# Optimization experiments

Hardware: AMD Instinct MI355X
Metric: run time of the kernel (lower is better)

Reference implementation:

```python
import jax, jax.numpy as jnp
import numpy as np
from jax import lax

_SIGMA = 1.5
_KSIZE = 5
_THRESH = 30.0
# TF rgb_to_grayscale luma weights
_RGB_W = np.array([0.2989, 0.5870, 0.1140], dtype=np.float32)

def _gauss1d():
    x = np.arange(_KSIZE, dtype=np.float32) - (_KSIZE - 1) / 2.0
    g = np.exp(-(x ** 2) / (2.0 * _SIGMA ** 2))
    return (g / g.sum()).astype(np.float32)

def _conv2d_same(x, k2d):
    # x: [B,H,W,1], k2d: [kh,kw]; reflect padding (TF image-op convention), valid conv
    kh, kw = k2d.shape
    ph, pw = kh // 2, kw // 2
    xp = jnp.pad(x, ((0, 0), (ph, ph), (pw, pw), (0, 0)), mode='reflect')
    k = k2d.reshape(kh, kw, 1, 1)
    return lax.conv_general_dilated(xp, k, window_strides=(1, 1), padding='VALID',
                                    dimension_numbers=('NHWC', 'HWIO', 'NHWC'))

def setup_inputs() -> dict:
    key = jax.random.key(0)
    inputs = jax.random.uniform(key, (32, 512, 512, 3), dtype=jnp.float32)
    return {"inputs": inputs}

def reference(inputs):
    # 1) grayscale
    gray = jnp.einsum('bhwc,c->bhw', inputs, jnp.asarray(_RGB_W))[..., None]  # [B,H,W,1]
    # 2) 5x5 gaussian blur (separable)
    g1 = jnp.asarray(_gauss1d())
    blurred = _conv2d_same(gray, g1[:, None])   # vertical pass [5,1]
    blurred = _conv2d_same(blurred, g1[None, :])  # horizontal pass [1,5]
    # 3) sobel x / y (3x3)
    kx = jnp.asarray(np.array([[-1, 0, 1], [-2, 0, 2], [-1, 0, 1]], dtype=np.float32))
    ky = jnp.asarray(np.array([[-1, -2, -1], [0, 0, 0], [1, 2, 1]], dtype=np.float32))
    sx = _conv2d_same(blurred, kx)
    sy = _conv2d_same(blurred, ky)
    # 4) magnitude + threshold (direction computed then unused in original; skipped)
    magnitude = jnp.sqrt(sx * sx + sy * sy)
    edges = jnp.where(magnitude > _THRESH, 1.0, 0.0).astype(inputs.dtype)
    return edges
```

## Files before the change

kernel.cpp:

```cpp
#include <hip/hip_runtime.h>

#define IMG_H 512
#define IMG_W 512
#define TILE  64
#define GR    70
#define GSTR  72
#define BR    66
#define BSTR  72
#define BLSTR 68

__device__ __forceinline__ int reflect(int i, int n) {
    i = (i < 0) ? -i : i;
    i = (i >= n) ? (2 * n - 2 - i) : i;
    return i;
}

__global__ __launch_bounds__(256)
void edge_fused_kernel(const float* __restrict__ in, float* __restrict__ out) {
    const int bx0 = blockIdx.x * TILE;
    const int by0 = blockIdx.y * TILE;
    const int b   = blockIdx.z;
    const int tx  = threadIdx.x;
    const int ty  = threadIdx.y;

    __shared__ float bufA[GR * GSTR];
    __shared__ float bufB[BR * BSTR];

    const float g0 = 0.12007839f;
    const float g1 = 0.23388075f;
    const float g2 = 0.29208172f;
    const float wr = 0.2989f, wg = 0.5870f, wb = 0.1140f;

    const float* img = in + (size_t)b * (IMG_H * IMG_W * 3);

    for (int i = ty; i < GR; i += 4) {
        const int gy = reflect(by0 - 3 + i, IMG_H);
        const float* row = img + (size_t)gy * (IMG_W * 3);
        for (int j = tx; j < GR; j += 64) {
            const int gx = reflect(bx0 - 3 + j, IMG_W);
            const float* p = row + gx * 3;
            bufA[i * GSTR + j] = p[0] * wr + p[1] * wg + p[2] * wb;
        }
    }
    __syncthreads();

    for (int i = ty; i < BR; i += 4) {
        for (int j = tx; j < GR; j += 64) {
            const float* c = &bufA[i * GSTR + j];
            bufB[i * BSTR + j] =
                g0 * (c[0] + c[4 * GSTR]) +
                g1 * (c[GSTR] + c[3 * GSTR]) +
                g2 * c[2 * GSTR];
        }
    }
    __syncthreads();

    for (int i = ty; i < BR; i += 4) {
        for (int j = tx; j < BR; j += 64) {
            const float* c = &bufB[i * BSTR + j];
            bufA[i * BLSTR + j] =
                g0 * (c[0] + c[4]) +
                g1 * (c[1] + c[3]) +
                g2 * c[2];
        }
    }
    __syncthreads();

    float* orow = out + (size_t)b * (IMG_H * IMG_W);
    for (int i = ty; i < TILE; i += 4) {
        const int oy = by0 + i;
        const int j = tx;
        const float* c = &bufA[(i + 1) * BLSTR + (j + 1)];
        const float tl = c[-BLSTR - 1], tc = c[-BLSTR], tr = c[-BLSTR + 1];
        const float ml = c[-1],                          mr = c[1];
        const float bl = c[BLSTR - 1],  bc = c[BLSTR],  br = c[BLSTR + 1];
        const float sx = (tr - tl) + 2.0f * (mr - ml) + (br - bl);
        const float sy = (bl - tl) + 2.0f * (bc - tc) + (br - tr);
        const float m2 = sx * sx + sy * sy;
        orow[(size_t)oy * IMG_W + bx0 + j] = (m2 > 900.0f) ? 1.0f : 0.0f;
    }
}

extern "C" void kernel_launch(void* const* d_in, const int* in_sizes, int n_in,
                              void* d_out, int out_size, void* d_ws, size_t ws_size,
                              hipStream_t stream) {
    const float* in = (const float*)d_in[0];
    float* out = (float*)d_out;
    const int B = in_sizes[0] / (IMG_H * IMG_W * 3);
    dim3 grid(IMG_W / TILE, IMG_H / TILE, B);
    dim3 block(64, 4, 1);
    edge_fused_kernel<<<grid, block, 0, stream>>>(in, out);
}
```

Before: 184.4 us.

## Vectorize fused edge kernel with float4 loads and smaller tiles

Replaces the scalar fused grayscale/blur/sobel kernel with a float4-vectorized version. Interior tiles load RGB with 128-bit global loads, the blur passes and the sobel stage use float4 shared-memory accesses, and the output is written as float4. Tiles shrink from 64x64 to 64x32 with a 1D block and a launch-bounds occupancy hint, which adds grid parallelism and raises the halo overhead. Edge tiles fall back to a scalar reflect path.

```diff
diff --git a/kernel.cpp b/kernel.cpp
--- a/kernel.cpp
+++ b/kernel.cpp
@@ -2,82 +2,122 @@
 
 #define IMG_H 512
 #define IMG_W 512
-#define TILE  64
-#define GR    70
-#define GSTR  72
-#define BR    66
-#define BSTR  72
-#define BLSTR 68
+#define TW 64
+#define TH 32
+#define GW 72
+#define GH 38
+#define GS 72
+#define TMH 34
+#define TMS 72
+#define BH 34
+#define BS 68
 
 __device__ __forceinline__ int reflect(int i, int n) {
     i = (i < 0) ? -i : i;
-    i = (i >= n) ? (2 * n - 2 - i) : i;
-    return i;
+    return (i >= n) ? (2 * n - 2 - i) : i;
 }
+__device__ __forceinline__ float4 ld4s(const float* p) { return *(const float4*)p; }
 
-__global__ __launch_bounds__(256)
+__global__ __launch_bounds__(256, 6)
 void edge_fused_kernel(const float* __restrict__ in, float* __restrict__ out) {
-    const int bx0 = blockIdx.x * TILE;
-    const int by0 = blockIdx.y * TILE;
+    const int bx0 = blockIdx.x * TW;
+    const int by0 = blockIdx.y * TH;
     const int b   = blockIdx.z;
-    const int tx  = threadIdx.x;
-    const int ty  = threadIdx.y;
+    const int tid = threadIdx.x;
 
-    __shared__ float bufA[GR * GSTR];
-    __shared__ float bufB[BR * BSTR];
+    __shared__ float A[GH * GS];
+    __shared__ float Bf[TMH * TMS + 8];
 
-    const float g0 = 0.12007839f;
-    const float g1 = 0.23388075f;
-    const float g2 = 0.29208172f;
+    const float g0 = 0.12007838f, g1 = 0.23388076f, g2 = 0.29208171f;
     const float wr = 0.2989f, wg = 0.5870f, wb = 0.1140f;
 
     const float* img = in + (size_t)b * (IMG_H * IMG_W * 3);
+    const int gx0 = bx0 - 4;
 
-    for (int i = ty; i < GR; i += 4) {
-        const int gy = reflect(by0 - 3 + i, IMG_H);
-        const float* row = img + (size_t)gy * (IMG_W * 3);
-        for (int j = tx; j < GR; j += 64) {
-            const int gx = reflect(bx0 - 3 + j, IMG_W);
-            const float* p = row + gx * 3;
-            bufA[i * GSTR + j] = p[0] * wr + p[1] * wg + p[2] * wb;
+    if (gx0 >= 0 && gx0 + GW <= IMG_W) {
+        for (int idx = tid; idx < GH * 18; idx += 256) {
+            const int i = idx / 18, g4 = idx % 18;
+            const int gy = reflect(by0 - 3 + i, IMG_H);
+            const float* rp = img + (size_t)gy * (IMG_W * 3) + (gx0 + 4 * g4) * 3;
+            const float4 v0 = ld4s(rp);
+            const float4 v1 = ld4s(rp + 4);
+            const float4 v2 = ld4s(rp + 8);
+            float4 g;
+            g.x = v0.x * wr + v0.y * wg + v0.z * wb;
+            g.y = v0.w * wr + v1.x * wg + v1.y * wb;
+            g.z = v1.z * wr + v1.w * wg + v2.x * wb;
+            g.w = v2.y * wr + v2.z * wg + v2.w * wb;
+            *(float4*)&A[i * GS + 4 * g4] = g;
+        }
+    } else {
+        for (int idx = tid; idx < GH * GW; idx += 256) {
+            const int i = idx / GW, j = idx % GW;
+            const int gy = reflect(by0 - 3 + i, IMG_H);
+            const int gx = reflect(gx0 + j, IMG_W);
+            const float* p = img + (size_t)gy * (IMG_W * 3) + gx * 3;
+            A[i * GS + j] = p[0] * wr + p[1] * wg + p[2] * wb;
         }
     }
     __syncthreads();
 
-    for (int i = ty; i < BR; i += 4) {
-        for (int j = tx; j < GR; j += 64) {
-            const float* c = &bufA[i * GSTR + j];
-            bufB[i * BSTR + j] =
-                g0 * (c[0] + c[4 * GSTR]) +
-                g1 * (c[GSTR] + c[3 * GSTR]) +
-                g2 * c[2 * GSTR];
-        }
+    for (int idx = tid; idx < TMH * 18; idx += 256) {
+        const int i = idx / 18, g4 = idx % 18;
+        const float* c = &A[i * GS + 4 * g4];
+        const float4 r0 = ld4s(c);
+        const float4 r1 = ld4s(c + GS);
+        const float4 r2 = ld4s(c + 2 * GS);
+        const float4 r3 = ld4s(c + 3 * GS);
+        const float4 r4 = ld4s(c + 4 * GS);
+        float4 t;
+        t.x = g0 * (r0.x + r4.x) + g1 * (r1.x + r3.x) + g2 * r2.x;
+        t.y = g0 * (r0.y + r4.y) + g1 * (r1.y + r3.y) + g2 * r2.y;
+        t.z = g0 * (r0.z + r4.z) + g1 * (r1.z + r3.z) + g2 * r2.z;
+        t.w = g0 * (r0.w + r4.w) + g1 * (r1.w + r3.w) + g2 * r2.w;
+        *(float4*)&Bf[i * TMS + 4 * g4] = t;
     }
     __syncthreads();
 
-    for (int i = ty; i < BR; i += 4) {
-        for (int j = tx; j < BR; j += 64) {
-            const float* c = &bufB[i * BSTR + j];
-            bufA[i * BLSTR + j] =
-                g0 * (c[0] + c[4]) +
-                g1 * (c[1] + c[3]) +
-                g2 * c[2];
-        }
+    for (int idx = tid; idx < BH * 17; idx += 256) {
+        const int i = idx / 17, g4 = idx % 17;
+        const float* c = &Bf[i * TMS + 4 * g4];
+        const float4 a = ld4s(c);
+        const float4 d = ld4s(c + 4);
+        const float4 e = ld4s(c + 8);
+        float4 o;
+        o.x = g0 * (a.y + d.y) + g1 * (a.z + d.x) + g2 * a.w;
+        o.y = g0 * (a.z + d.z) + g1 * (a.w + d.y) + g2 * d.x;
+        o.z = g0 * (a.w + d.w) + g1 * (d.x + d.z) + g2 * d.y;
+        o.w = g0 * (d.x + e.x) + g1 * (d.y + d.w) + g2 * d.z;
+        *(float4*)&A[i * BS + 4 * g4] = o;
     }
     __syncthreads();
 
-    float* orow = out + (size_t)b * (IMG_H * IMG_W);
-    for (int i = ty; i < TILE; i += 4) {
-        const int oy = by0 + i;
-        const int j = tx;
-        const float* c = &bufA[(i + 1) * BLSTR + (j + 1)];
-        const float tl = c[-BLSTR - 1], tc = c[-BLSTR], tr = c[-BLSTR + 1];
-        const float ml = c[-1],                          mr = c[1];
-        const float bl = c[BLSTR - 1],  bc = c[BLSTR],  br = c[BLSTR + 1];
-        const float sx = (tr - tl) + 2.0f * (mr - ml) + (br - bl);
-        const float sy = (bl - tl) + 2.0f * (bc - tc) + (br - tr);
-        const float m2 = sx * sx + sy * sy;
-        orow[(size_t)oy * IMG_W + bx0 + j] = (m2 > 900.0f) ? 1.0f : 0.0f;
+    const int xg = tid & 15;
+    const int x  = xg * 4;
+    float* ob = out + (size_t)b * (IMG_H * IMG_W) + (size_t)by0 * IMG_W + bx0;
+    for (int y = tid >> 4; y < TH; y += 16) {
+        const float* r0 = &A[y * BS + x];
+        float t[8], m[8], bo[8];
+        float4 q;
+        q = ld4s(r0);          t[0]=q.x; t[1]=q.y; t[2]=q.z; t[3]=q.w;
+        q = ld4s(r0 + 4);      t[4]=q.x; t[5]=q.y; t[6]=q.z; t[7]=q.w;
+        q = ld4s(r0 + BS);     m[0]=q.x; m[1]=q.y; m[2]=q.z; m[3]=q.w;
+        q = ld4s(r0 + BS + 4); m[4]=q.x; m[5]=q.y; m[6]=q.z; m[7]=q.w;
+        q = ld4s(r0 + 2*BS);   bo[0]=q.x; bo[1]=q.y; bo[2]=q.z; bo[3]=q.w;
+        q = ld4s(r0 + 2*BS+4); bo[4]=q.x; bo[5]=q.y; bo[6]=q.z; bo[7]=q.w;
+        float res[4];
+        #pragma unroll
+        for (int k = 0; k < 4; ++k) {
+            const float tl = t[k],  tc = t[k+1],  tr = t[k+2];
+            const float ml = m[k],                 mr = m[k+2];
+            const float bl = bo[k], bc = bo[k+1], br = bo[k+2];
+            const float sx = (tr - tl) + 2.0f * (mr - ml) + (br - bl);
+            const float sy = (bl - tl) + 2.0f * (bc - tc) + (br - tr);
+            const float m2 = sx * sx + sy * sy;
+            res[k] = (m2 > 900.0f) ? 1.0f : 0.0f;
+        }
+        float4 rv; rv.x = res[0]; rv.y = res[1]; rv.z = res[2]; rv.w = res[3];
+        *(float4*)&ob[(size_t)y * IMG_W + x] = rv;
     }
 }
 
@@ -87,7 +127,7 @@
     const float* in = (const float*)d_in[0];
     float* out = (float*)d_out;
     const int B = in_sizes[0] / (IMG_H * IMG_W * 3);
-    dim3 grid(IMG_W / TILE, IMG_H / TILE, B);
-    dim3 block(64, 4, 1);
+    dim3 grid(IMG_W / TW, IMG_H / TH, B);
+    dim3 block(256, 1, 1);
     edge_fused_kernel<<<grid, block, 0, stream>>>(in, out);
 }
```

Result: faster. 161.7 us (-12.3%).

## Rewrite edge kernel with composed blur-Sobel taps, vector loads and prefetch

Applied to the files above, without the earlier changes.

Folds the Gaussian blur and Sobel operators algebraically into two separable 7-tap filters, applied vertically then horizontally. Reads RGB with float4 vector loads and computes grayscale four pixels at a time. Splits each block into two 32-row halves, prefetching the second half's input into registers while the first half is computed, and writes output as float4. Reflect boundaries are handled through templated edge modes. The changes cut redundant shared-memory passes and scalar global loads, but add register pressure and boundary-handling complexity.

```diff
diff --git a/kernel.cpp b/kernel.cpp
--- a/kernel.cpp
+++ b/kernel.cpp
@@ -2,83 +2,181 @@
 
 #define IMG_H 512
 #define IMG_W 512
-#define TILE  64
-#define GR    70
-#define GSTR  72
-#define BR    66
-#define BSTR  72
-#define BLSTR 68
+#define TW 64
+#define TH 32
+#define GH 38
+#define AS 72
+#define VS 72
 
 __device__ __forceinline__ int reflect(int i, int n) {
     i = (i < 0) ? -i : i;
-    i = (i >= n) ? (2 * n - 2 - i) : i;
-    return i;
+    return (i >= n) ? (2 * n - 2 - i) : i;
+}
+__device__ __forceinline__ float4 ld4s(const float* p) { return *(const float4*)p; }
+
+struct RGB9 { float4 a0,a1,a2,b0,b1,b2,c0,c1,c2; };
+
+__device__ __forceinline__ const float* rgbptr(const float* img, int by0, int i, int gx0, int j) {
+    const int gy = reflect(by0 - 3 + i, IMG_H);
+    return img + (size_t)gy * (IMG_W * 3) + (gx0 + 4 * j) * 3;
 }
 
-__global__ __launch_bounds__(256)
-void edge_fused_kernel(const float* __restrict__ in, float* __restrict__ out) {
-    const int bx0 = blockIdx.x * TILE;
-    const int by0 = blockIdx.y * TILE;
-    const int b   = blockIdx.z;
-    const int tx  = threadIdx.x;
-    const int ty  = threadIdx.y;
+template<int D, int GO, int N>
+__device__ __forceinline__ void issue_loads(const float* img, int by0, int gx0, int tid, RGB9& r) {
+    const int i0 = tid / D,         j0 = tid % D + GO;
+    const int i1 = (tid+256) / D,   j1 = (tid+256) % D + GO;
+    int idx2 = tid + 512; if (idx2 >= N) idx2 = N - 1;
+    const int i2 = idx2 / D,        j2 = idx2 % D + GO;
+    const float* p0 = rgbptr(img, by0, i0, gx0, j0);
+    const float* p1 = rgbptr(img, by0, i1, gx0, j1);
+    const float* p2 = rgbptr(img, by0, i2, gx0, j2);
+    r.a0 = ld4s(p0); r.a1 = ld4s(p0+4); r.a2 = ld4s(p0+8);
+    r.b0 = ld4s(p1); r.b1 = ld4s(p1+4); r.b2 = ld4s(p1+8);
+    r.c0 = ld4s(p2); r.c1 = ld4s(p2+4); r.c2 = ld4s(p2+8);
+}
 
-    __shared__ float bufA[GR * GSTR];
-    __shared__ float bufB[BR * BSTR];
+#define GRAY4F(v0, v1, v2, dst) do { \
+    float4 g_; \
+    g_.x = (v0).x * 0.2989f + (v0).y * 0.5870f + (v0).z * 0.1140f; \
+    g_.y = (v0).w * 0.2989f + (v1).x * 0.5870f + (v1).y * 0.1140f; \
+    g_.z = (v1).z * 0.2989f + (v1).w * 0.5870f + (v2).x * 0.1140f; \
+    g_.w = (v2).y * 0.2989f + (v2).z * 0.5870f + (v2).w * 0.1140f; \
+    *(float4*)(dst) = g_; \
+} while (0)
 
-    const float g0 = 0.12007839f;
-    const float g1 = 0.23388075f;
-    const float g2 = 0.29208172f;
-    const float wr = 0.2989f, wg = 0.5870f, wb = 0.1140f;
+template<int D, int GO, int N>
+__device__ __forceinline__ void gray_store(float* A, const RGB9& r, int tid) {
+    {
+        const int i = tid / D, j = tid % D + GO;
+        GRAY4F(r.a0, r.a1, r.a2, &A[i * AS + 4 * j]);
+    }
+    {
+        const int i = (tid+256) / D, j = (tid+256) % D + GO;
+        GRAY4F(r.b0, r.b1, r.b2, &A[i * AS + 4 * j]);
+    }
+    if (tid + 512 < N) {
+        const int i = (tid+512) / D, j = (tid+512) % D + GO;
+        GRAY4F(r.c0, r.c1, r.c2, &A[i * AS + 4 * j]);
+    }
+}
 
-    const float* img = in + (size_t)b * (IMG_H * IMG_W * 3);
-
-    for (int i = ty; i < GR; i += 4) {
-        const int gy = reflect(by0 - 3 + i, IMG_H);
-        const float* row = img + (size_t)gy * (IMG_W * 3);
-        for (int j = tx; j < GR; j += 64) {
-            const int gx = reflect(bx0 - 3 + j, IMG_W);
-            const float* p = row + gx * 3;
-            bufA[i * GSTR + j] = p[0] * wr + p[1] * wg + p[2] * wb;
+template<int BMODE>
+__device__ __forceinline__ void vtaps(const float* A, float* B1, float* B2, int tid) {
+    const float C1[7] = { 0.12007838f, 0.47403752f, 0.87992161f, 1.05192494f,
+                          0.87992161f, 0.47403752f, 0.12007838f };
+    const float C2[7] = { -0.12007838f, -0.23388076f, -0.17200333f, 0.0f,
+                           0.17200333f,  0.23388076f,  0.12007838f };
+    #pragma unroll
+    for (int s = 0; s < 2; ++s) {
+        if (s == 1 && tid >= 32) break;
+        const int idx = tid + 256 * s;
+        const int rq = idx / 18, g = idx % 18;
+        const bool bnd = (BMODE == 1 && g == 0) || (BMODE == 2 && g == 17);
+        float p1[2][4] = {{0,0,0,0},{0,0,0,0}};
+        float p2[2][4] = {{0,0,0,0},{0,0,0,0}};
+        #pragma unroll
+        for (int k = 0; k < 8; ++k) {
+            const int row = 2 * rq + k;
+            float x[4];
+            if (!bnd) {
+                const float4 q = ld4s(&A[row * AS + 4 * g]);
+                x[0]=q.x; x[1]=q.y; x[2]=q.z; x[3]=q.w;
+            } else if (BMODE == 1) {
+                x[0]=A[row*AS+8]; x[1]=A[row*AS+7]; x[2]=A[row*AS+6]; x[3]=A[row*AS+5];
+            } else {
+                x[0]=A[row*AS+66]; x[1]=A[row*AS+65]; x[2]=A[row*AS+64]; x[3]=A[row*AS+63];
+            }
+            if (k < 7) {
+                #pragma unroll
+                for (int c = 0; c < 4; ++c) {
+                    p1[0][c] = fmaf(C1[k], x[c], p1[0][c]);
+                    if (k != 3) p2[0][c] = fmaf(C2[k], x[c], p2[0][c]);
+                }
+            }
+            if (k > 0) {
+                #pragma unroll
+                for (int c = 0; c < 4; ++c) {
+                    p1[1][c] = fmaf(C1[k-1], x[c], p1[1][c]);
+                    if (k != 4) p2[1][c] = fmaf(C2[k-1], x[c], p2[1][c]);
+                }
+            }
+        }
+        #pragma unroll
+        for (int o = 0; o < 2; ++o) {
+            float4 w1, w2;
+            w1.x=p1[o][0]; w1.y=p1[o][1]; w1.z=p1[o][2]; w1.w=p1[o][3];
+            w2.x=p2[o][0]; w2.y=p2[o][1]; w2.z=p2[o][2]; w2.w=p2[o][3];
+            *(float4*)&B1[(2*rq+o)*VS + 4*g] = w1;
+            *(float4*)&B2[(2*rq+o)*VS + 4*g] = w2;
         }
     }
+}
+
+__device__ __forceinline__ void htaps_store(const float* B1, const float* B2,
+                                            float* outB, int by0, int bx0, int tid) {
+    const float a1 = 0.17200333f, a2 = 0.23388076f, a3 = 0.12007838f;
+    const float c0 = 1.05192494f, c1 = 0.87992161f, c2 = 0.47403752f, c3 = 0.12007838f;
+    #pragma unroll
+    for (int t = 0; t < 2; ++t) {
+        const int idx = tid + 256 * t;
+        const int r = idx >> 4, g = idx & 15;
+        const float* q1 = &B1[r * VS + 4 * g];
+        const float* q2 = &B2[r * VS + 4 * g];
+        float u[12], w[12];
+        float4 v;
+        v = ld4s(q1);    u[0]=v.x; u[1]=v.y; u[2]=v.z; u[3]=v.w;
+        v = ld4s(q1+4);  u[4]=v.x; u[5]=v.y; u[6]=v.z; u[7]=v.w;
+        v = ld4s(q1+8);  u[8]=v.x; u[9]=v.y; u[10]=v.z; u[11]=v.w;
+        v = ld4s(q2);    w[0]=v.x; w[1]=v.y; w[2]=v.z; w[3]=v.w;
+        v = ld4s(q2+4);  w[4]=v.x; w[5]=v.y; w[6]=v.z; w[7]=v.w;
+        v = ld4s(q2+8);  w[8]=v.x; w[9]=v.y; w[10]=v.z; w[11]=v.w;
+        float res[4];
+        #pragma unroll
+        for (int p = 0; p < 4; ++p) {
+            const int j = p + 4;
+            const float sx = (u[j+3]-u[j-3])*a3 + (u[j+2]-u[j-2])*a2 + (u[j+1]-u[j-1])*a1;
+            const float sy = c0*w[j] + c1*(w[j-1]+w[j+1]) + c2*(w[j-2]+w[j+2]) + c3*(w[j-3]+w[j+3]);
+            res[p] = (sx*sx + sy*sy > 900.0f) ? 1.0f : 0.0f;
+        }
+        float4 rv; rv.x=res[0]; rv.y=res[1]; rv.z=res[2]; rv.w=res[3];
+        *(float4*)&outB[(size_t)(by0 + r) * IMG_W + bx0 + 4*g] = rv;
+    }
+}
+
+template<int D, int GO, int N, int BMODE>
+__device__ __forceinline__ void run_block(const float* img, float* outB,
+                                          int bx0, int byB, int tid,
+                                          float* A, float* B1, float* B2) {
+    const int gx0 = bx0 - 4;
+    RGB9 rA, rB;
+    issue_loads<D,GO,N>(img, byB, gx0, tid, rA);
+    gray_store<D,GO,N>(A, rA, tid);
     __syncthreads();
+    issue_loads<D,GO,N>(img, byB + TH, gx0, tid, rB);
+    vtaps<BMODE>(A, B1, B2, tid);
+    __syncthreads();
+    htaps_store(B1, B2, outB, byB, bx0, tid);
+    gray_store<D,GO,N>(A, rB, tid);
+    __syncthreads();
+    vtaps<BMODE>(A, B1, B2, tid);
+    __syncthreads();
+    htaps_store(B1, B2, outB, byB + TH, bx0, tid);
+}
 
-    for (int i = ty; i < BR; i += 4) {
-        for (int j = tx; j < GR; j += 64) {
-            const float* c = &bufA[i * GSTR + j];
-            bufB[i * BSTR + j] =
-                g0 * (c[0] + c[4 * GSTR]) +
-                g1 * (c[GSTR] + c[3 * GSTR]) +
-                g2 * c[2 * GSTR];
-        }
-    }
-    __syncthreads();
-
-    for (int i = ty; i < BR; i += 4) {
-        for (int j = tx; j < BR; j += 64) {
-            const float* c = &bufB[i * BSTR + j];
-            bufA[i * BLSTR + j] =
-                g0 * (c[0] + c[4]) +
-                g1 * (c[1] + c[3]) +
-                g2 * c[2];
-        }
-    }
-    __syncthreads();
-
-    float* orow = out + (size_t)b * (IMG_H * IMG_W);
-    for (int i = ty; i < TILE; i += 4) {
-        const int oy = by0 + i;
-        const int j = tx;
-        const float* c = &bufA[(i + 1) * BLSTR + (j + 1)];
-        const float tl = c[-BLSTR - 1], tc = c[-BLSTR], tr = c[-BLSTR + 1];
-        const float ml = c[-1],                          mr = c[1];
-        const float bl = c[BLSTR - 1],  bc = c[BLSTR],  br = c[BLSTR + 1];
-        const float sx = (tr - tl) + 2.0f * (mr - ml) + (br - bl);
-        const float sy = (bl - tl) + 2.0f * (bc - tc) + (br - tr);
-        const float m2 = sx * sx + sy * sy;
-        orow[(size_t)oy * IMG_W + bx0 + j] = (m2 > 900.0f) ? 1.0f : 0.0f;
-    }
+__global__ __launch_bounds__(256, 4)
+void edge_fused_kernel(const float* __restrict__ in, float* __restrict__ out) {
+    const int bx0 = blockIdx.x * TW;
+    const int byB = blockIdx.y * (2 * TH);
+    const int b   = blockIdx.z;
+    const int tid = threadIdx.x;
+    __shared__ float A[GH * AS];
+    __shared__ float B1[TH * VS];
+    __shared__ float B2[TH * VS];
+    const float* img = in + (size_t)b * (IMG_H * IMG_W * 3);
+    float* outB = out + (size_t)b * (IMG_H * IMG_W);
+    if (bx0 == 0)                    run_block<17,1,646,1>(img, outB, bx0, byB, tid, A, B1, B2);
+    else if (bx0 + TW == IMG_W)      run_block<17,0,646,2>(img, outB, bx0, byB, tid, A, B1, B2);
+    else                             run_block<18,0,684,0>(img, outB, bx0, byB, tid, A, B1, B2);
 }
 
 extern "C" void kernel_launch(void* const* d_in, const int* in_sizes, int n_in,
@@ -87,7 +185,7 @@
     const float* in = (const float*)d_in[0];
     float* out = (float*)d_out;
     const int B = in_sizes[0] / (IMG_H * IMG_W * 3);
-    dim3 grid(IMG_W / TILE, IMG_H / TILE, B);
-    dim3 block(64, 4, 1);
+    dim3 grid(IMG_W / TW, IMG_H / (2 * TH), B);
+    dim3 block(256, 1, 1);
     edge_fused_kernel<<<grid, block, 0, stream>>>(in, out);
 }
```

Measured after the change: 157.5 us. 1.17x faster.

## Replace shared-memory tiled pipeline with single-wave register sliding window and merged 7-tap filters

Applied to the files above, without the earlier changes.

Each 64-lane wavefront handles a 58-column band and walks down a 64-row strip. It keeps a 7-row rolling window of grayscale values in registers and folds the Gaussian blur and Sobel operators into merged 7-tap separable filters, with the horizontal taps done via lane shuffles. This removes the LDS staging, the barriers and the separate blur passes. In exchange, halo columns are recomputed across bands, some lanes are wasted at the band edges, and each block holds only one wave, which may lower occupancy or latency hiding. Folding the blur into the Sobel taps is exact only where reflect padding of the blurred image matches reflecting the raw input, so boundary pixels may differ from the reference.

```diff
diff --git a/kernel.cpp b/kernel.cpp
--- a/kernel.cpp
+++ b/kernel.cpp
@@ -2,82 +2,69 @@
 
 #define IMG_H 512
 #define IMG_W 512
-#define TILE  64
-#define GR    70
-#define GSTR  72
-#define BR    66
-#define BSTR  72
-#define BLSTR 68
+#define BAND   58
+#define STRIPH 64
 
-__device__ __forceinline__ int reflect(int i, int n) {
-    i = (i < 0) ? -i : i;
-    i = (i >= n) ? (2 * n - 2 - i) : i;
-    return i;
-}
+__global__ __launch_bounds__(64)
+void edge_wave_kernel(const float* __restrict__ in, float* __restrict__ out) {
+    const int band = blockIdx.x;
+    const int y0   = blockIdx.y * STRIPH;
+    const int img  = blockIdx.z;
+    const int lane = threadIdx.x;
 
-__global__ __launch_bounds__(256)
-void edge_fused_kernel(const float* __restrict__ in, float* __restrict__ out) {
-    const int bx0 = blockIdx.x * TILE;
-    const int by0 = blockIdx.y * TILE;
-    const int b   = blockIdx.z;
-    const int tx  = threadIdx.x;
-    const int ty  = threadIdx.y;
+    const int col = band * BAND - 3 + lane;
+    int rc = col < 0 ? -col : col;
+    rc = rc >= IMG_W ? (2 * IMG_W - 2 - rc) : rc;
+    const bool valid = (lane >= 3) && (lane < 3 + BAND) && (col < IMG_W);
 
-    __shared__ float bufA[GR * GSTR];
-    __shared__ float bufB[BR * BSTR];
+    const float* src = in + (size_t)img * (IMG_H * IMG_W * 3) + (size_t)rc * 3;
+    float* dst = out + (size_t)img * (IMG_H * IMG_W) + (size_t)y0 * IMG_W + col;
 
-    const float g0 = 0.12007839f;
-    const float g1 = 0.23388075f;
-    const float g2 = 0.29208172f;
     const float wr = 0.2989f, wg = 0.5870f, wb = 0.1140f;
+    const float c0 = 1.05192494f, c1 = 0.87992161f, c2 = 0.47403752f, c3 = 0.12007838f;
+    const float a1 = 0.17200333f, a2 = 0.23388076f, a3 = 0.12007838f;
 
-    const float* img = in + (size_t)b * (IMG_H * IMG_W * 3);
+    float w[7];
 
-    for (int i = ty; i < GR; i += 4) {
-        const int gy = reflect(by0 - 3 + i, IMG_H);
-        const float* row = img + (size_t)gy * (IMG_W * 3);
-        for (int j = tx; j < GR; j += 64) {
-            const int gx = reflect(bx0 - 3 + j, IMG_W);
-            const float* p = row + gx * 3;
-            bufA[i * GSTR + j] = p[0] * wr + p[1] * wg + p[2] * wb;
+    auto grayrow = [&](int l) -> float {
+        int y = y0 - 3 + l;
+        y = y < 0 ? -y : y;
+        y = y >= IMG_H ? (2 * IMG_H - 2 - y) : y;
+        const float* p = src + (size_t)y * (IMG_W * 3);
+        return p[0] * wr + p[1] * wg + p[2] * wb;
+    };
+
+    auto emit = [&](int r, int o) {
+        const float wA = w[o % 7],       wB = w[(o + 1) % 7], wC = w[(o + 2) % 7],
+                    wD = w[(o + 3) % 7], wE = w[(o + 4) % 7], wF = w[(o + 5) % 7],
+                    wG = w[(o + 6) % 7];
+        const float v1 = c3 * (wA + wG) + c2 * (wB + wF) + c1 * (wC + wE) + c0 * wD;
+        const float v2 = a3 * (wG - wA) + a2 * (wF - wB) + a1 * (wE - wC);
+
+        const float v1m1 = __shfl_up(v1, 1, 64), v1p1 = __shfl_down(v1, 1, 64);
+        const float v1m2 = __shfl_up(v1, 2, 64), v1p2 = __shfl_down(v1, 2, 64);
+        const float v1m3 = __shfl_up(v1, 3, 64), v1p3 = __shfl_down(v1, 3, 64);
+        const float v2m1 = __shfl_up(v2, 1, 64), v2p1 = __shfl_down(v2, 1, 64);
+        const float v2m2 = __shfl_up(v2, 2, 64), v2p2 = __shfl_down(v2, 2, 64);
+        const float v2m3 = __shfl_up(v2, 3, 64), v2p3 = __shfl_down(v2, 3, 64);
+
+        const float sx = a1 * (v1p1 - v1m1) + a2 * (v1p2 - v1m2) + a3 * (v1p3 - v1m3);
+        const float sy = c0 * v2 + c1 * (v2p1 + v2m1) + c2 * (v2p2 + v2m2) + c3 * (v2p3 + v2m3);
+        const float m2 = sx * sx + sy * sy;
+        if (valid) dst[(size_t)r * IMG_W] = (m2 > 900.0f) ? 1.0f : 0.0f;
+    };
+
+    #pragma unroll
+    for (int l = 0; l < 7; ++l) w[l] = grayrow(l);
+    emit(0, 0);
+
+    for (int c = 0; c < 9; ++c) {
+        const int lb = 7 * c + 7;
+        #pragma unroll
+        for (int k = 0; k < 7; ++k) {
+            w[k] = grayrow(lb + k);
+            emit(7 * c + 1 + k, (k + 1) % 7);
         }
-    }
-    __syncthreads();
-
-    for (int i = ty; i < BR; i += 4) {
-        for (int j = tx; j < GR; j += 64) {
-            const float* c = &bufA[i * GSTR + j];
-            bufB[i * BSTR + j] =
-                g0 * (c[0] + c[4 * GSTR]) +
-                g1 * (c[GSTR] + c[3 * GSTR]) +
-                g2 * c[2 * GSTR];
-        }
-    }
-    __syncthreads();
-
-    for (int i = ty; i < BR; i += 4) {
-        for (int j = tx; j < BR; j += 64) {
-            const float* c = &bufB[i * BSTR + j];
-            bufA[i * BLSTR + j] =
-                g0 * (c[0] + c[4]) +
-                g1 * (c[1] + c[3]) +
-                g2 * c[2];
-        }
-    }
-    __syncthreads();
-
-    float* orow = out + (size_t)b * (IMG_H * IMG_W);
-    for (int i = ty; i < TILE; i += 4) {
-        const int oy = by0 + i;
-        const int j = tx;
-        const float* c = &bufA[(i + 1) * BLSTR + (j + 1)];
-        const float tl = c[-BLSTR - 1], tc = c[-BLSTR], tr = c[-BLSTR + 1];
-        const float ml = c[-1],                          mr = c[1];
-        const float bl = c[BLSTR - 1],  bc = c[BLSTR],  br = c[BLSTR + 1];
-        const float sx = (tr - tl) + 2.0f * (mr - ml) + (br - bl);
-        const float sy = (bl - tl) + 2.0f * (bc - tc) + (br - tr);
-        const float m2 = sx * sx + sy * sy;
-        orow[(size_t)oy * IMG_W + bx0 + j] = (m2 > 900.0f) ? 1.0f : 0.0f;
     }
 }
 
@@ -87,7 +74,8 @@
     const float* in = (const float*)d_in[0];
     float* out = (float*)d_out;
     const int B = in_sizes[0] / (IMG_H * IMG_W * 3);
-    dim3 grid(IMG_W / TILE, IMG_H / TILE, B);
-    dim3 block(64, 4, 1);
-    edge_fused_kernel<<<grid, block, 0, stream>>>(in, out);
+    const int nbands = (IMG_W + BAND - 1) / BAND;
+    dim3 grid(nbands, IMG_H / STRIPH, B);
+    dim3 block(64, 1, 1);
+    edge_wave_kernel<<<grid, block, 0, stream>>>(in, out);
 }
```

After: 179.6 us. 1.03x faster.
